# Performance work log

Measured on AMD Instinct MI355X. Metric: run time of the kernel, lower is better.

## Reference

```python
import jax, jax.numpy as jnp
import numpy as np

LAMBDA_DRO = 0.1
EPSILON = 0.5
EPS = 1e-8

N, M, D, K = 2048, 4096, 512, 1000


def _cosine_matrix(a, b):
    # a: [N, d], b: [M, d] -> [N, M] cosine similarity via normalize + GEMM
    an = a / jnp.maximum(jnp.linalg.norm(a, axis=1, keepdims=True), EPS)
    bn = b / jnp.maximum(jnp.linalg.norm(b, axis=1, keepdims=True), EPS)
    return an @ bn.T


def setup_inputs() -> dict:
    key = jax.random.key(0)
    k = jax.random.split(key, 7)
    return {
        "ptr_features": jax.random.normal(k[0], (N, D), dtype=jnp.float32),
        "ptr_logits": jax.random.normal(k[1], (N, K), dtype=jnp.float32),
        "ptr_labels": jax.random.randint(k[2], (N,), 0, K),
        "nu_features": jax.random.normal(k[3], (M, D), dtype=jnp.float32),
        "nu_logits": jax.random.normal(k[4], (M, K), dtype=jnp.float32),
        "nu_labels": jax.random.randint(k[5], (M,), 0, K),
        "classifier_weights": jax.random.normal(k[6], (K, D), dtype=jnp.float32),
    }


def reference(ptr_features, ptr_logits, ptr_labels, nu_features, nu_logits,
              nu_labels, classifier_weights):
    # per-sample CE loss on nu (hard labels)
    log_probs = jax.nn.log_softmax(nu_logits, axis=1)          # [M, K]
    nu_losses = -jnp.take_along_axis(log_probs, nu_labels[:, None], axis=1)[:, 0]  # [M]

    # transport costs
    C_X = 1.0 - _cosine_matrix(ptr_features, nu_features)       # [N, M]
    ptr_emb = classifier_weights[ptr_labels]                    # [N, d]
    nu_emb = classifier_weights[nu_labels]                      # [M, d]
    C_Y = 1.0 - _cosine_matrix(ptr_emb, nu_emb)                 # [N, M]
    C_total = C_X + C_Y

    # worst-case distribution Q^lambda
    exponent = (nu_losses[None, :] - LAMBDA_DRO * C_total) / (LAMBDA_DRO * EPSILON + EPS)
    exponent = exponent - jnp.max(exponent, axis=1, keepdims=True)
    exp_terms = jnp.exp(exponent)                               # [N, M]
    weights = exp_terms / (jnp.sum(exp_terms, axis=1, keepdims=True) + EPS)
    probs = jnp.mean(weights, axis=0)                           # [M]
    probs = probs / (jnp.sum(probs) + EPS)

    dro_loss = jnp.sum(probs * nu_losses)
    total_loss = dro_loss  # semantic_loss = 0 (no moco inputs)
    return (total_loss, dro_loss, probs, jnp.mean(C_total), jnp.mean(C_X), jnp.mean(C_Y))
```

## Files before the change

kernel.cpp:

```cpp
#include <hip/hip_runtime.h>
#include <math.h>

#define N_PTR 2048
#define M_NU  4096
#define DIM   512
#define KCLS  1000
#define KPAD  1024

static constexpr float LAMBDA_ = 0.1f;
static constexpr float EPS_ = 1e-8f;
static constexpr float INV_DENOM = 1.0f / (0.1f * 0.5f + 1e-8f);

typedef short short8 __attribute__((ext_vector_type(8)));
typedef unsigned short u16x8 __attribute__((ext_vector_type(8)));
typedef float f32x4 __attribute__((ext_vector_type(4)));

__device__ __forceinline__ unsigned short f2bf(float x) {
  unsigned u = __float_as_uint(x);
  u += 0x7fff + ((u >> 16) & 1);
  return (unsigned short)(u >> 16);
}
__device__ __forceinline__ float bf2f(unsigned short h) {
  return __uint_as_float(((unsigned)h) << 16);
}

__device__ __forceinline__ void gload16(const void* g, void* l) {
  __builtin_amdgcn_global_load_lds(
      (const __attribute__((address_space(1))) unsigned int*)g,
      (__attribute__((address_space(3))) unsigned int*)l, 16, 0, 0);
}

__device__ __forceinline__ float blk_reduce_sum(float v, float* red) {
  #pragma unroll
  for (int off = 32; off > 0; off >>= 1) v += __shfl_down(v, off);
  __syncthreads();
  if ((threadIdx.x & 63) == 0) red[threadIdx.x >> 6] = v;
  __syncthreads();
  return red[0] + red[1] + red[2] + red[3];
}

__device__ __forceinline__ float blk_reduce_max(float v, float* red) {
  #pragma unroll
  for (int off = 32; off > 0; off >>= 1) v = fmaxf(v, __shfl_down(v, off));
  __syncthreads();
  if ((threadIdx.x & 63) == 0) red[threadIdx.x >> 6] = v;
  __syncthreads();
  return fmaxf(fmaxf(red[0], red[1]), fmaxf(red[2], red[3]));
}

__global__ __launch_bounds__(256) void prep_kernel(
    const float* __restrict__ ptr_f, const float* __restrict__ nu_f,
    const float* __restrict__ cls_f, const float* __restrict__ logits,
    const int* __restrict__ labels, unsigned short* __restrict__ An,
    unsigned short* __restrict__ Bn, unsigned short* __restrict__ Cn,
    float* __restrict__ losses) {
  __shared__ float red[4];
  int b = blockIdx.x;
  if (b < 1792) {
    int gid = b * 256 + threadIdx.x;
    int row = gid >> 6, lane = gid & 63;
    const float* src; unsigned short* dst; int lrow; int in_rows;
    if (row < N_PTR)             { src = ptr_f; dst = An; lrow = row;                in_rows = N_PTR; }
    else if (row < N_PTR + M_NU) { src = nu_f;  dst = Bn; lrow = row - N_PTR;        in_rows = M_NU; }
    else                         { src = cls_f; dst = Cn; lrow = row - N_PTR - M_NU; in_rows = KCLS; }
    u16x8 ov;
    if (lrow < in_rows) {
      const float4* rp = (const float4*)(src + (size_t)lrow * DIM);
      float4 a = rp[lane * 2], bq = rp[lane * 2 + 1];
      float v[8] = {a.x, a.y, a.z, a.w, bq.x, bq.y, bq.z, bq.w};
      float s = 0.f;
      #pragma unroll
      for (int j = 0; j < 8; ++j) s = fmaf(v[j], v[j], s);
      #pragma unroll
      for (int off = 32; off > 0; off >>= 1) s += __shfl_xor(s, off);
      float inv = 1.0f / fmaxf(sqrtf(s), EPS_);
      #pragma unroll
      for (int j = 0; j < 8; ++j) ov[j] = f2bf(v[j] * inv);
    } else {
      #pragma unroll
      for (int j = 0; j < 8; ++j) ov[j] = 0;
    }
    *(u16x8*)(dst + (size_t)lrow * DIM + lane * 8) = ov;
  } else {
    int row = b - 1792;
    int tid = threadIdx.x;
    const float* x = logits + (size_t)row * KCLS;
    const float4* x4 = (const float4*)x;
    float4 v = make_float4(0.f, 0.f, 0.f, 0.f);
    float mx_loc = -INFINITY;
    if (tid < 250) {
      v = x4[tid];
      mx_loc = fmaxf(fmaxf(v.x, v.y), fmaxf(v.z, v.w));
    }
    float mx = blk_reduce_max(mx_loc, red);
    float se_loc = 0.f;
    if (tid < 250)
      se_loc = __expf(v.x - mx) + __expf(v.y - mx) + __expf(v.z - mx) + __expf(v.w - mx);
    float se = blk_reduce_sum(se_loc, red);
    if (tid == 0) losses[row] = mx + logf(se) - x[labels[row]];
  }
}

template <int BM, int MODE>
__global__ __launch_bounds__(256) void mfma_gemm(
    const unsigned short* __restrict__ A, const unsigned short* __restrict__ B,
    unsigned short* __restrict__ Gfb, unsigned short* __restrict__ Tb,
    const int* __restrict__ pl, const int* __restrict__ nl,
    const float* __restrict__ nu_loss, unsigned* __restrict__ gbits,
    float* __restrict__ pr, float* __restrict__ pr2,
    float* __restrict__ s_part, float* __restrict__ gy_part, int ldc) {
  constexpr int FR = BM / 32;
  constexpr int WSPAN = BM / 2;
  __shared__ unsigned short Alds[BM * 64];
  __shared__ unsigned short Blds[BM * 64];
  __shared__ float red[4];
  const int tid = threadIdx.x;
  const int w = tid >> 6, lane = tid & 63;
  const int brow = blockIdx.y * BM, bcol = blockIdx.x * BM;
  const int wr = w >> 1, wc = w & 1;

  if (MODE == 0 && blockIdx.x == 0 && blockIdx.y == 0) {
    float mloc = 0.f;
    for (int i = tid; i < M_NU; i += 256) mloc = fmaxf(mloc, nu_loss[i]);
    float mx = blk_reduce_max(mloc, red);
    if (tid == 0) *gbits = __float_as_uint(mx);
    __syncthreads();
  }

  const int sr = lane >> 3;
  const int sc = lane & 7;
  const int schunk = (sc ^ sr) * 8;

  f32x4 acc[FR][FR] = {};

  for (int k0 = 0; k0 < DIM; k0 += 64) {
    #pragma unroll
    for (int i = 0; i < FR; ++i) {
      int j = w * FR + i;
      int r = j * 8 + sr;
      gload16(A + (size_t)(brow + r) * DIM + k0 + schunk, (char*)Alds + j * 1024);
      gload16(B + (size_t)(bcol + r) * DIM + k0 + schunk, (char*)Blds + j * 1024);
    }
    __syncthreads();
    #pragma unroll
    for (int kk = 0; kk < 2; ++kk) {
      const int koff = kk * 64 + (lane >> 4) * 16;
      short8 af[FR], bfr[FR];
      #pragma unroll
      for (int mi = 0; mi < FR; ++mi) {
        int r = wr * WSPAN + mi * 16 + (lane & 15);
        af[mi] = *(const short8*)((const char*)Alds + r * 128 + (koff ^ ((r & 7) << 4)));
      }
      #pragma unroll
      for (int ni = 0; ni < FR; ++ni) {
        int r = wc * WSPAN + ni * 16 + (lane & 15);
        bfr[ni] = *(const short8*)((const char*)Blds + r * 128 + (koff ^ ((r & 7) << 4)));
      }
      #pragma unroll
      for (int mi = 0; mi < FR; ++mi)
        #pragma unroll
        for (int ni = 0; ni < FR; ++ni)
          acc[mi][ni] = __builtin_amdgcn_mfma_f32_16x16x32_bf16(af[mi], bfr[ni], acc[mi][ni], 0, 0, 0);
    }
    __syncthreads();
  }

  if (MODE == 0) {
    #pragma unroll
    for (int mi = 0; mi < FR; ++mi)
      #pragma unroll
      for (int ni = 0; ni < FR; ++ni)
        #pragma unroll
        for (int j = 0; j < 4; ++j) {
          int row = brow + wr * WSPAN + mi * 16 + (lane >> 4) * 4 + j;
          int col = bcol + wc * WSPAN + ni * 16 + (lane & 15);
          Gfb[(size_t)row * ldc + col] = f2bf(acc[mi][ni][j]);
        }
  } else {
    const float gmax = __uint_as_float(*gbits);
    const float fac = LAMBDA_ * INV_DENOM;
    int cols[FR]; float a_r[FR]; float loss_r[FR]; int nl_r[FR];
    #pragma unroll
    for (int ni = 0; ni < FR; ++ni) {
      cols[ni]  = bcol + wc * WSPAN + ni * 16 + (lane & 15);
      loss_r[ni] = nu_loss[cols[ni]];
      a_r[ni]   = (loss_r[ni] - gmax - 2.f * LAMBDA_) * INV_DENOM;
      nl_r[ni]  = nl[cols[ni]];
    }
    float s_acc = 0.f, gy_acc = 0.f;
    #pragma unroll
    for (int mi = 0; mi < FR; ++mi) {
      #pragma unroll
      for (int j = 0; j < 4; ++j) {
        int row = brow + wr * WSPAN + mi * 16 + (lane >> 4) * 4 + j;
        const unsigned short* Grow = Gfb + (size_t)pl[row] * KPAD;
        float rowacc = 0.f, rowacc2 = 0.f;
        #pragma unroll
        for (int ni = 0; ni < FR; ++ni) {
          float s  = acc[mi][ni][j];
          float gy = bf2f(Grow[nl_r[ni]]);
          float e  = fmaf(fac, s + gy, a_r[ni]);
          float t  = __expf(e);
          unsigned short tb = f2bf(t);
          Tb[(size_t)row * ldc + cols[ni]] = tb;
          float tt = bf2f(tb);
          rowacc  += tt;
          rowacc2 += tt * loss_r[ni];
          s_acc += s; gy_acc += gy;
        }
        #pragma unroll
        for (int off = 1; off < 16; off <<= 1) {
          rowacc  += __shfl_xor(rowacc, off);
          rowacc2 += __shfl_xor(rowacc2, off);
        }
        if ((lane & 15) == 0) {
          pr [(size_t)(blockIdx.x * 2 + wc) * N_PTR + row] = rowacc;
          pr2[(size_t)(blockIdx.x * 2 + wc) * N_PTR + row] = rowacc2;
        }
      }
    }
    float stot = blk_reduce_sum(s_acc, red);
    float gtot = blk_reduce_sum(gy_acc, red);
    if (tid == 0) {
      int bid = blockIdx.y * gridDim.x + blockIdx.x;
      s_part[bid] = stot; gy_part[bid] = gtot;
    }
  }
}

__global__ __launch_bounds__(256) void colpass_td_kernel(
    const unsigned short* __restrict__ Tb, const float* __restrict__ pr,
    const float* __restrict__ pr2, float* __restrict__ partial,
    float* __restrict__ T_part, float* __restrict__ D_part) {
  __shared__ float sh[64];
  int b = blockIdx.x, tid = threadIdx.x;
  if (b < 256) {
    int bx = b & 7, by = b >> 3;
    int m0 = bx * 512 + tid * 2;
    int n0 = by * 64;
    if (tid < 64) {
      float rs = 0.f;
      #pragma unroll 4
      for (int cb = 0; cb < 64; ++cb) rs += pr[(size_t)cb * N_PTR + n0 + tid];
      sh[tid] = 1.0f / (rs + EPS_);
    }
    __syncthreads();
    float a0 = 0.f, a1 = 0.f;
    #pragma unroll 4
    for (int i = 0; i < 64; ++i) {
      unsigned tv = *(const unsigned*)(Tb + (size_t)(n0 + i) * M_NU + m0);
      float wv = sh[i];
      a0 = fmaf(bf2f((unsigned short)(tv & 0xffffu)), wv, a0);
      a1 = fmaf(bf2f((unsigned short)(tv >> 16)), wv, a1);
    }
    *(float2*)(partial + (size_t)by * M_NU + m0) = make_float2(a0, a1);
  } else {
    int n = (b - 256) * 128 + (tid & 127);
    float tl = 0.f, dl = 0.f;
    if (tid < 128) {
      float rs = 0.f, wl = 0.f;
      #pragma unroll 4
      for (int cb = 0; cb < 64; ++cb) {
        rs += pr [(size_t)cb * N_PTR + n];
        wl += pr2[(size_t)cb * N_PTR + n];
      }
      float wi = 1.0f / (rs + EPS_);
      tl = rs * wi; dl = wl * wi;
    }
    __syncthreads();
    #pragma unroll
    for (int off = 32; off > 0; off >>= 1) { tl += __shfl_down(tl, off); dl += __shfl_down(dl, off); }
    if ((tid & 63) == 0) { sh[tid >> 6] = tl; sh[4 + (tid >> 6)] = dl; }
    __syncthreads();
    if (tid == 0) {
      T_part[b - 256] = sh[0] + sh[1] + sh[2] + sh[3];
      D_part[b - 256] = sh[4] + sh[5] + sh[6] + sh[7];
    }
  }
}

__global__ __launch_bounds__(256) void final_kernel(const float* __restrict__ partial,
    const float* __restrict__ T_part, const float* __restrict__ D_part,
    const float* __restrict__ s_part, const float* __restrict__ gy_part,
    float* __restrict__ out) {
  __shared__ float red[4];
  int b = blockIdx.x, tid = threadIdx.x;
  float T = 0.f;
  #pragma unroll
  for (int i = 0; i < 16; ++i) T += T_part[i];
  float scale = (1.0f / (float)N_PTR) / (T / (float)N_PTR + EPS_);
  if (b < 16) {
    int m = b * 256 + tid;
    float raw = 0.f;
    #pragma unroll
    for (int c = 0; c < 32; ++c) raw += partial[(size_t)c * M_NU + m];
    out[2 + m] = raw * scale;
  } else {
    float D = 0.f;
    #pragma unroll
    for (int i = 0; i < 16; ++i) D += D_part[i];
    float ls = 0.f, lg = 0.f;
    for (int i = tid; i < 512; i += 256) { ls += s_part[i]; lg += gy_part[i]; }
    float S  = blk_reduce_sum(ls, red);
    float Gy = blk_reduce_sum(lg, red);
    if (tid == 0) {
      float dro = D * scale;
      const float invNM = 1.0f / ((float)N_PTR * (float)M_NU);
      float mcx = 1.f - S * invNM;
      float mcy = 1.f - Gy * invNM;
      out[0] = dro;
      out[1] = dro;
      out[2 + M_NU] = mcx + mcy;
      out[3 + M_NU] = mcx;
      out[4 + M_NU] = mcy;
    }
  }
}

extern "C" void kernel_launch(void* const* d_in, const int* in_sizes, int n_in,
                              void* d_out, int out_size, void* d_ws, size_t ws_size,
                              hipStream_t stream) {
  const float* ptr_feat = (const float*)d_in[0];
  const int*   ptr_lab  = (const int*)d_in[2];
  const float* nu_feat  = (const float*)d_in[3];
  const float* nu_log   = (const float*)d_in[4];
  const int*   nu_lab   = (const int*)d_in[5];
  const float* cls_w    = (const float*)d_in[6];
  float* out = (float*)d_out;

  char* base = (char*)d_ws;
  unsigned short* Tb  = (unsigned short*)base;
  unsigned short* Gfb = (unsigned short*)(base + 16u * 1024 * 1024);
  unsigned short* An  = (unsigned short*)(base + 18u * 1024 * 1024);
  unsigned short* Bn  = (unsigned short*)(base + 20u * 1024 * 1024);
  unsigned short* Cn  = (unsigned short*)(base + 24u * 1024 * 1024);
  float* fb           = (float*)(base + 25u * 1024 * 1024);
  float* nloss   = fb;
  unsigned* gbits= (unsigned*)(nloss + 4096);
  float* pr      = nloss + 4096 + 64;
  float* pr2     = pr  + 64 * N_PTR;
  float* partial = pr2 + 64 * N_PTR;
  float* s_part  = partial + 32 * M_NU;
  float* gy_part = s_part + 512;
  float* T_part  = gy_part + 512;
  float* D_part  = T_part + 16;

  prep_kernel<<<dim3(1792 + M_NU), 256, 0, stream>>>(
      ptr_feat, nu_feat, cls_w, nu_log, nu_lab, An, Bn, Cn, nloss);
  mfma_gemm<64, 0><<<dim3(KPAD / 64, KPAD / 64), 256, 0, stream>>>(
      Cn, Cn, Gfb, nullptr, nullptr, nullptr, nloss, gbits,
      nullptr, nullptr, nullptr, nullptr, KPAD);
  mfma_gemm<128, 1><<<dim3(M_NU / 128, N_PTR / 128), 256, 0, stream>>>(
      An, Bn, Gfb, Tb, ptr_lab, nu_lab, nloss, gbits,
      pr, pr2, s_part, gy_part, M_NU);
  colpass_td_kernel<<<dim3(272), 256, 0, stream>>>(Tb, pr, pr2, partial, T_part, D_part);
  final_kernel<<<dim3(17), 256, 0, stream>>>(partial, T_part, D_part, s_part, gy_part, out);
}
```

Before: 62.79 us.

## Transpose MFMA output layout for vectorized stores and use wave-per-row softmax

The MFMA operands are swapped so each lane holds four consecutive columns of one row. The GEMM epilogues can then write packed 4-element bf16 stores instead of scattered 2-byte stores, and each row's partial sums need only two cross-lane shuffles. Separately, the per-row cross-entropy now runs one wavefront per row, four rows per block, using only wave shuffles and no block barriers. The cost is more per-lane registers for the per-column loss and label arrays, and gather reads of Gfb that are now per-row rather than per-column.

Result: slower. 79.67 us (+26.9%).

```diff
diff --git a/kernel.cpp b/kernel.cpp
--- a/kernel.cpp
+++ b/kernel.cpp
@@ -13,6 +13,7 @@
 
 typedef short short8 __attribute__((ext_vector_type(8)));
 typedef unsigned short u16x8 __attribute__((ext_vector_type(8)));
+typedef unsigned short u16x4 __attribute__((ext_vector_type(4)));
 typedef float f32x4 __attribute__((ext_vector_type(4)));
 
 __device__ __forceinline__ unsigned short f2bf(float x) {
@@ -54,10 +55,10 @@
     const int* __restrict__ labels, unsigned short* __restrict__ An,
     unsigned short* __restrict__ Bn, unsigned short* __restrict__ Cn,
     float* __restrict__ losses) {
-  __shared__ float red[4];
   int b = blockIdx.x;
+  int tid = threadIdx.x;
   if (b < 1792) {
-    int gid = b * 256 + threadIdx.x;
+    int gid = b * 256 + tid;
     int row = gid >> 6, lane = gid & 63;
     const float* src; unsigned short* dst; int lrow; int in_rows;
     if (row < N_PTR)             { src = ptr_f; dst = An; lrow = row;                in_rows = N_PTR; }
@@ -82,22 +83,27 @@
     }
     *(u16x8*)(dst + (size_t)lrow * DIM + lane * 8) = ov;
   } else {
-    int row = b - 1792;
-    int tid = threadIdx.x;
-    const float* x = logits + (size_t)row * KCLS;
-    const float4* x4 = (const float4*)x;
-    float4 v = make_float4(0.f, 0.f, 0.f, 0.f);
-    float mx_loc = -INFINITY;
-    if (tid < 250) {
-      v = x4[tid];
-      mx_loc = fmaxf(fmaxf(v.x, v.y), fmaxf(v.z, v.w));
-    }
-    float mx = blk_reduce_max(mx_loc, red);
-    float se_loc = 0.f;
-    if (tid < 250)
-      se_loc = __expf(v.x - mx) + __expf(v.y - mx) + __expf(v.z - mx) + __expf(v.w - mx);
-    float se = blk_reduce_sum(se_loc, red);
-    if (tid == 0) losses[row] = mx + logf(se) - x[labels[row]];
+    int row = (b - 1792) * 4 + (tid >> 6);
+    int lane = tid & 63;
+    const float4* x4 = (const float4*)(logits + (size_t)row * KCLS);
+    float4 v0 = x4[lane], v1 = x4[lane + 64], v2 = x4[lane + 128];
+    bool has3 = lane < 58;
+    float4 v3 = has3 ? x4[lane + 192] : make_float4(0.f, 0.f, 0.f, 0.f);
+    float mx = fmaxf(fmaxf(fmaxf(v0.x, v0.y), fmaxf(v0.z, v0.w)),
+               fmaxf(fmaxf(fmaxf(v1.x, v1.y), fmaxf(v1.z, v1.w)),
+                     fmaxf(fmaxf(v2.x, v2.y), fmaxf(v2.z, v2.w))));
+    if (has3) mx = fmaxf(mx, fmaxf(fmaxf(v3.x, v3.y), fmaxf(v3.z, v3.w)));
+    #pragma unroll
+    for (int off = 32; off > 0; off >>= 1) mx = fmaxf(mx, __shfl_xor(mx, off));
+    float se = __expf(v0.x - mx) + __expf(v0.y - mx) + __expf(v0.z - mx) + __expf(v0.w - mx)
+             + __expf(v1.x - mx) + __expf(v1.y - mx) + __expf(v1.z - mx) + __expf(v1.w - mx)
+             + __expf(v2.x - mx) + __expf(v2.y - mx) + __expf(v2.z - mx) + __expf(v2.w - mx);
+    if (has3)
+      se += __expf(v3.x - mx) + __expf(v3.y - mx) + __expf(v3.z - mx) + __expf(v3.w - mx);
+    #pragma unroll
+    for (int off = 32; off > 0; off >>= 1) se += __shfl_xor(se, off);
+    if (lane == 0)
+      losses[row] = mx + logf(se) - logits[(size_t)row * KCLS + labels[row]];
   }
 }
 
@@ -160,63 +166,66 @@
       for (int mi = 0; mi < FR; ++mi)
         #pragma unroll
         for (int ni = 0; ni < FR; ++ni)
-          acc[mi][ni] = __builtin_amdgcn_mfma_f32_16x16x32_bf16(af[mi], bfr[ni], acc[mi][ni], 0, 0, 0);
+          acc[mi][ni] = __builtin_amdgcn_mfma_f32_16x16x32_bf16(bfr[ni], af[mi], acc[mi][ni], 0, 0, 0);
     }
     __syncthreads();
   }
 
   if (MODE == 0) {
     #pragma unroll
-    for (int mi = 0; mi < FR; ++mi)
-      #pragma unroll
-      for (int ni = 0; ni < FR; ++ni)
+    for (int mi = 0; mi < FR; ++mi) {
+      int n = brow + wr * WSPAN + mi * 16 + (lane & 15);
+      #pragma unroll
+      for (int ni = 0; ni < FR; ++ni) {
+        int mb = bcol + wc * WSPAN + ni * 16 + ((lane >> 4) << 2);
+        u16x4 o;
         #pragma unroll
-        for (int j = 0; j < 4; ++j) {
-          int row = brow + wr * WSPAN + mi * 16 + (lane >> 4) * 4 + j;
-          int col = bcol + wc * WSPAN + ni * 16 + (lane & 15);
-          Gfb[(size_t)row * ldc + col] = f2bf(acc[mi][ni][j]);
-        }
+        for (int j = 0; j < 4; ++j) o[j] = f2bf(acc[mi][ni][j]);
+        *(u16x4*)(Gfb + (size_t)n * ldc + mb) = o;
+      }
+    }
   } else {
     const float gmax = __uint_as_float(*gbits);
     const float fac = LAMBDA_ * INV_DENOM;
-    int cols[FR]; float a_r[FR]; float loss_r[FR]; int nl_r[FR];
-    #pragma unroll
-    for (int ni = 0; ni < FR; ++ni) {
-      cols[ni]  = bcol + wc * WSPAN + ni * 16 + (lane & 15);
-      loss_r[ni] = nu_loss[cols[ni]];
-      a_r[ni]   = (loss_r[ni] - gmax - 2.f * LAMBDA_) * INV_DENOM;
-      nl_r[ni]  = nl[cols[ni]];
-    }
+    float a_r[FR][4]; float l_r[FR][4]; int nl_r[FR][4];
+    #pragma unroll
+    for (int ni = 0; ni < FR; ++ni)
+      #pragma unroll
+      for (int j = 0; j < 4; ++j) {
+        int m = bcol + wc * WSPAN + ni * 16 + ((lane >> 4) << 2) + j;
+        float l = nu_loss[m];
+        l_r[ni][j]  = l;
+        a_r[ni][j]  = (l - gmax - 2.f * LAMBDA_) * INV_DENOM;
+        nl_r[ni][j] = nl[m];
+      }
     float s_acc = 0.f, gy_acc = 0.f;
     #pragma unroll
     for (int mi = 0; mi < FR; ++mi) {
-      #pragma unroll
-      for (int j = 0; j < 4; ++j) {
-        int row = brow + wr * WSPAN + mi * 16 + (lane >> 4) * 4 + j;
-        const unsigned short* Grow = Gfb + (size_t)pl[row] * KPAD;
-        float rowacc = 0.f, rowacc2 = 0.f;
+      int n = brow + wr * WSPAN + mi * 16 + (lane & 15);
+      const unsigned short* Grow = Gfb + (size_t)pl[n] * KPAD;
+      float ra = 0.f, ra2 = 0.f;
+      #pragma unroll
+      for (int ni = 0; ni < FR; ++ni) {
+        int mb = bcol + wc * WSPAN + ni * 16 + ((lane >> 4) << 2);
+        u16x4 o;
         #pragma unroll
-        for (int ni = 0; ni < FR; ++ni) {
+        for (int j = 0; j < 4; ++j) {
           float s  = acc[mi][ni][j];
-          float gy = bf2f(Grow[nl_r[ni]]);
-          float e  = fmaf(fac, s + gy, a_r[ni]);
-          float t  = __expf(e);
-          unsigned short tb = f2bf(t);
-          Tb[(size_t)row * ldc + cols[ni]] = tb;
-          float tt = bf2f(tb);
-          rowacc  += tt;
-          rowacc2 += tt * loss_r[ni];
+          float gy = bf2f(Grow[nl_r[ni][j]]);
+          float t  = __expf(fmaf(fac, s + gy, a_r[ni][j]));
+          o[j] = f2bf(t);
+          float tt = bf2f(o[j]);
+          ra  += tt;
+          ra2 += tt * l_r[ni][j];
           s_acc += s; gy_acc += gy;
         }
-        #pragma unroll
-        for (int off = 1; off < 16; off <<= 1) {
-          rowacc  += __shfl_xor(rowacc, off);
-          rowacc2 += __shfl_xor(rowacc2, off);
-        }
-        if ((lane & 15) == 0) {
-          pr [(size_t)(blockIdx.x * 2 + wc) * N_PTR + row] = rowacc;
-          pr2[(size_t)(blockIdx.x * 2 + wc) * N_PTR + row] = rowacc2;
-        }
+        *(u16x4*)(Tb + (size_t)n * ldc + mb) = o;
+      }
+      ra  += __shfl_xor(ra, 16);  ra  += __shfl_xor(ra, 32);
+      ra2 += __shfl_xor(ra2, 16); ra2 += __shfl_xor(ra2, 32);
+      if (lane < 16) {
+        pr [(size_t)(blockIdx.x * 2 + wc) * N_PTR + n] = ra;
+        pr2[(size_t)(blockIdx.x * 2 + wc) * N_PTR + n] = ra2;
       }
     }
     float stot = blk_reduce_sum(s_acc, red);
@@ -345,7 +354,7 @@
   float* T_part  = gy_part + 512;
   float* D_part  = T_part + 16;
 
-  prep_kernel<<<dim3(1792 + M_NU), 256, 0, stream>>>(
+  prep_kernel<<<dim3(1792 + M_NU / 4), 256, 0, stream>>>(
       ptr_feat, nu_feat, cls_w, nu_log, nu_lab, An, Bn, Cn, nloss);
   mfma_gemm<64, 0><<<dim3(KPAD / 64, KPAD / 64), 256, 0, stream>>>(
       Cn, Cn, Gfb, nullptr, nullptr, nullptr, nloss, gbits,
```

## Split big GEMM epilogue into a separate row pass and compute means via column sums

Applied to the files above, without the earlier changes.

The big feature GEMM now only writes bf16 similarities with vectorized transposed stores. A new row-pass kernel reads them back with the class-embedding row cached in LDS, computes the exp terms and row sums, and overwrites them in place. The means of C_X and C_Y are now computed from column sums of the normalized embeddings (sum of dot products equals the dot product of sums), in extra blocks of the small GEMM, replacing the per-element accumulation. This drops gather and exp work from the GEMM epilogue, but it adds one more kernel launch and an extra read and write of the N×M bf16 matrix.

Result: slower. 102.5 us (+63.3%).

```diff
diff --git a/kernel.cpp b/kernel.cpp
--- a/kernel.cpp
+++ b/kernel.cpp
@@ -13,6 +13,7 @@
 
 typedef short short8 __attribute__((ext_vector_type(8)));
 typedef unsigned short u16x8 __attribute__((ext_vector_type(8)));
+typedef unsigned short u16x4 __attribute__((ext_vector_type(4)));
 typedef float f32x4 __attribute__((ext_vector_type(4)));
 
 __device__ __forceinline__ unsigned short f2bf(float x) {
@@ -56,8 +57,9 @@
     float* __restrict__ losses) {
   __shared__ float red[4];
   int b = blockIdx.x;
+  int tid = threadIdx.x;
   if (b < 1792) {
-    int gid = b * 256 + threadIdx.x;
+    int gid = b * 256 + tid;
     int row = gid >> 6, lane = gid & 63;
     const float* src; unsigned short* dst; int lrow; int in_rows;
     if (row < N_PTR)             { src = ptr_f; dst = An; lrow = row;                in_rows = N_PTR; }
@@ -83,7 +85,6 @@
     *(u16x8*)(dst + (size_t)lrow * DIM + lane * 8) = ov;
   } else {
     int row = b - 1792;
-    int tid = threadIdx.x;
     const float* x = logits + (size_t)row * KCLS;
     const float4* x4 = (const float4*)x;
     float4 v = make_float4(0.f, 0.f, 0.f, 0.f);
@@ -101,31 +102,54 @@
   }
 }
 
-template <int BM, int MODE>
-__global__ __launch_bounds__(256) void mfma_gemm(
+template <int BM, int GX, int EXTRA>
+__global__ __launch_bounds__(256) void gemm_kernel(
     const unsigned short* __restrict__ A, const unsigned short* __restrict__ B,
-    unsigned short* __restrict__ Gfb, unsigned short* __restrict__ Tb,
+    unsigned short* __restrict__ C, int ldc,
+    const unsigned short* __restrict__ An, const unsigned short* __restrict__ Bn,
+    const unsigned short* __restrict__ Cn,
     const int* __restrict__ pl, const int* __restrict__ nl,
-    const float* __restrict__ nu_loss, unsigned* __restrict__ gbits,
-    float* __restrict__ pr, float* __restrict__ pr2,
-    float* __restrict__ s_part, float* __restrict__ gy_part, int ldc) {
+    const float* __restrict__ nloss, float* __restrict__ csum_part,
+    unsigned* __restrict__ gbits) {
   constexpr int FR = BM / 32;
   constexpr int WSPAN = BM / 2;
+  constexpr int NTILES = GX * 16;
+  const int b = blockIdx.x;
+  const int tid = threadIdx.x;
+
+  if (EXTRA && b >= NTILES) {
+    int j = b - NTILES;
+    __shared__ float red[4];
+    if (j == 96) {
+      float mloc = 0.f;
+      for (int i = tid; i < M_NU; i += 256) mloc = fmaxf(mloc, nloss[i]);
+      float mx = blk_reduce_max(mloc, red);
+      if (tid == 0) *gbits = __float_as_uint(mx);
+      return;
+    }
+    const unsigned short* basep; const int* idx = nullptr; int n0;
+    if (j < 16)      { basep = An; n0 = j * 128; }
+    else if (j < 48) { basep = Bn; n0 = (j - 16) * 128; }
+    else if (j < 64) { basep = Cn; idx = pl; n0 = (j - 48) * 128; }
+    else             { basep = Cn; idx = nl; n0 = (j - 64) * 128; }
+    float a0 = 0.f, a1 = 0.f;
+    for (int i = 0; i < 128; ++i) {
+      int rr = n0 + i;
+      const unsigned short* rowp = basep + (size_t)(idx ? idx[rr] : rr) * DIM;
+      unsigned v = *(const unsigned*)(rowp + tid * 2);
+      a0 += bf2f((unsigned short)(v & 0xffffu));
+      a1 += bf2f((unsigned short)(v >> 16));
+    }
+    csum_part[(size_t)j * DIM + tid * 2]     = a0;
+    csum_part[(size_t)j * DIM + tid * 2 + 1] = a1;
+    return;
+  }
+
   __shared__ unsigned short Alds[BM * 64];
   __shared__ unsigned short Blds[BM * 64];
-  __shared__ float red[4];
-  const int tid = threadIdx.x;
   const int w = tid >> 6, lane = tid & 63;
-  const int brow = blockIdx.y * BM, bcol = blockIdx.x * BM;
+  const int bcol = (b % GX) * BM, brow = (b / GX) * BM;
   const int wr = w >> 1, wc = w & 1;
-
-  if (MODE == 0 && blockIdx.x == 0 && blockIdx.y == 0) {
-    float mloc = 0.f;
-    for (int i = tid; i < M_NU; i += 256) mloc = fmaxf(mloc, nu_loss[i]);
-    float mx = blk_reduce_max(mloc, red);
-    if (tid == 0) *gbits = __float_as_uint(mx);
-    __syncthreads();
-  }
 
   const int sr = lane >> 3;
   const int sc = lane & 7;
@@ -160,134 +184,122 @@
       for (int mi = 0; mi < FR; ++mi)
         #pragma unroll
         for (int ni = 0; ni < FR; ++ni)
-          acc[mi][ni] = __builtin_amdgcn_mfma_f32_16x16x32_bf16(af[mi], bfr[ni], acc[mi][ni], 0, 0, 0);
+          acc[mi][ni] = __builtin_amdgcn_mfma_f32_16x16x32_bf16(bfr[ni], af[mi], acc[mi][ni], 0, 0, 0);
     }
     __syncthreads();
   }
 
-  if (MODE == 0) {
-    #pragma unroll
-    for (int mi = 0; mi < FR; ++mi)
-      #pragma unroll
-      for (int ni = 0; ni < FR; ++ni)
-        #pragma unroll
-        for (int j = 0; j < 4; ++j) {
-          int row = brow + wr * WSPAN + mi * 16 + (lane >> 4) * 4 + j;
-          int col = bcol + wc * WSPAN + ni * 16 + (lane & 15);
-          Gfb[(size_t)row * ldc + col] = f2bf(acc[mi][ni][j]);
-        }
-  } else {
-    const float gmax = __uint_as_float(*gbits);
-    const float fac = LAMBDA_ * INV_DENOM;
-    int cols[FR]; float a_r[FR]; float loss_r[FR]; int nl_r[FR];
+  #pragma unroll
+  for (int mi = 0; mi < FR; ++mi) {
+    int n = brow + wr * WSPAN + mi * 16 + (lane & 15);
     #pragma unroll
     for (int ni = 0; ni < FR; ++ni) {
-      cols[ni]  = bcol + wc * WSPAN + ni * 16 + (lane & 15);
-      loss_r[ni] = nu_loss[cols[ni]];
-      a_r[ni]   = (loss_r[ni] - gmax - 2.f * LAMBDA_) * INV_DENOM;
-      nl_r[ni]  = nl[cols[ni]];
-    }
-    float s_acc = 0.f, gy_acc = 0.f;
-    #pragma unroll
-    for (int mi = 0; mi < FR; ++mi) {
-      #pragma unroll
-      for (int j = 0; j < 4; ++j) {
-        int row = brow + wr * WSPAN + mi * 16 + (lane >> 4) * 4 + j;
-        const unsigned short* Grow = Gfb + (size_t)pl[row] * KPAD;
-        float rowacc = 0.f, rowacc2 = 0.f;
-        #pragma unroll
-        for (int ni = 0; ni < FR; ++ni) {
-          float s  = acc[mi][ni][j];
-          float gy = bf2f(Grow[nl_r[ni]]);
-          float e  = fmaf(fac, s + gy, a_r[ni]);
-          float t  = __expf(e);
-          unsigned short tb = f2bf(t);
-          Tb[(size_t)row * ldc + cols[ni]] = tb;
-          float tt = bf2f(tb);
-          rowacc  += tt;
-          rowacc2 += tt * loss_r[ni];
-          s_acc += s; gy_acc += gy;
-        }
-        #pragma unroll
-        for (int off = 1; off < 16; off <<= 1) {
-          rowacc  += __shfl_xor(rowacc, off);
-          rowacc2 += __shfl_xor(rowacc2, off);
-        }
-        if ((lane & 15) == 0) {
-          pr [(size_t)(blockIdx.x * 2 + wc) * N_PTR + row] = rowacc;
-          pr2[(size_t)(blockIdx.x * 2 + wc) * N_PTR + row] = rowacc2;
-        }
-      }
-    }
-    float stot = blk_reduce_sum(s_acc, red);
-    float gtot = blk_reduce_sum(gy_acc, red);
-    if (tid == 0) {
-      int bid = blockIdx.y * gridDim.x + blockIdx.x;
-      s_part[bid] = stot; gy_part[bid] = gtot;
-    }
-  }
-}
-
-__global__ __launch_bounds__(256) void colpass_td_kernel(
-    const unsigned short* __restrict__ Tb, const float* __restrict__ pr,
-    const float* __restrict__ pr2, float* __restrict__ partial,
-    float* __restrict__ T_part, float* __restrict__ D_part) {
-  __shared__ float sh[64];
+      int mb = bcol + wc * WSPAN + ni * 16 + ((lane >> 4) << 2);
+      u16x4 o;
+      #pragma unroll
+      for (int j = 0; j < 4; ++j) o[j] = f2bf(acc[mi][ni][j]);
+      *(u16x4*)(C + (size_t)n * ldc + mb) = o;
+    }
+  }
+}
+
+__global__ __launch_bounds__(256) void rowpass_kernel(
+    unsigned short* __restrict__ Sb, const unsigned short* __restrict__ Gfb,
+    const int* __restrict__ pl, const int* __restrict__ nl,
+    const float* __restrict__ nloss, const unsigned* __restrict__ gbits,
+    float* __restrict__ winv, float* __restrict__ trow, float* __restrict__ drow) {
+  __shared__ unsigned short Gld[4][KPAD];
+  const int wv = threadIdx.x >> 6, lane = threadIdx.x & 63;
+  const int n = blockIdx.x * 4 + wv;
+  const float gmax = __uint_as_float(*gbits);
+  const float fac = LAMBDA_ * INV_DENOM;
+  const float csh = gmax + 2.f * LAMBDA_;
+  const unsigned short* Grow = Gfb + (size_t)pl[n] * KPAD;
+  *(u16x8*)(&Gld[wv][lane * 16])     = *(const u16x8*)(Grow + lane * 16);
+  *(u16x8*)(&Gld[wv][lane * 16 + 8]) = *(const u16x8*)(Grow + lane * 16 + 8);
+  __syncthreads();
+  unsigned short* Srow = Sb + (size_t)n * M_NU;
+  float rs = 0.f, rl = 0.f;
+  #pragma unroll
+  for (int it = 0; it < 4; ++it) {
+    const int m0 = it * 1024 + lane * 16;
+    u16x8 s0 = *(const u16x8*)(Srow + m0);
+    u16x8 s1 = *(const u16x8*)(Srow + m0 + 8);
+    int4 n0v = *(const int4*)(nl + m0);
+    int4 n1v = *(const int4*)(nl + m0 + 4);
+    int4 n2v = *(const int4*)(nl + m0 + 8);
+    int4 n3v = *(const int4*)(nl + m0 + 12);
+    float4 l0 = *(const float4*)(nloss + m0);
+    float4 l1 = *(const float4*)(nloss + m0 + 4);
+    float4 l2 = *(const float4*)(nloss + m0 + 8);
+    float4 l3 = *(const float4*)(nloss + m0 + 12);
+    const int nli[16] = {n0v.x, n0v.y, n0v.z, n0v.w, n1v.x, n1v.y, n1v.z, n1v.w,
+                         n2v.x, n2v.y, n2v.z, n2v.w, n3v.x, n3v.y, n3v.z, n3v.w};
+    const float li[16] = {l0.x, l0.y, l0.z, l0.w, l1.x, l1.y, l1.z, l1.w,
+                          l2.x, l2.y, l2.z, l2.w, l3.x, l3.y, l3.z, l3.w};
+    u16x8 t0, t1;
+    #pragma unroll
+    for (int j = 0; j < 8; ++j) {
+      float gy = bf2f(Gld[wv][nli[j]]);
+      float t  = __expf(fmaf(fac, bf2f(s0[j]) + gy, (li[j] - csh) * INV_DENOM));
+      t0[j] = f2bf(t);
+      float tt = bf2f(t0[j]);
+      rs += tt; rl += tt * li[j];
+    }
+    #pragma unroll
+    for (int j = 0; j < 8; ++j) {
+      float gy = bf2f(Gld[wv][nli[8 + j]]);
+      float t  = __expf(fmaf(fac, bf2f(s1[j]) + gy, (li[8 + j] - csh) * INV_DENOM));
+      t1[j] = f2bf(t);
+      float tt = bf2f(t1[j]);
+      rs += tt; rl += tt * li[8 + j];
+    }
+    *(u16x8*)(Srow + m0)     = t0;
+    *(u16x8*)(Srow + m0 + 8) = t1;
+  }
+  #pragma unroll
+  for (int off = 32; off > 0; off >>= 1) {
+    rs += __shfl_xor(rs, off);
+    rl += __shfl_xor(rl, off);
+  }
+  if (lane == 0) {
+    float wi = 1.0f / (rs + EPS_);
+    winv[n] = wi;
+    trow[n] = rs * wi;
+    drow[n] = rl * wi;
+  }
+}
+
+__global__ __launch_bounds__(256) void colpass_kernel(
+    const unsigned short* __restrict__ Tb, const float* __restrict__ winv,
+    float* __restrict__ partial) {
+  __shared__ float w[64];
   int b = blockIdx.x, tid = threadIdx.x;
-  if (b < 256) {
-    int bx = b & 7, by = b >> 3;
-    int m0 = bx * 512 + tid * 2;
-    int n0 = by * 64;
-    if (tid < 64) {
-      float rs = 0.f;
-      #pragma unroll 4
-      for (int cb = 0; cb < 64; ++cb) rs += pr[(size_t)cb * N_PTR + n0 + tid];
-      sh[tid] = 1.0f / (rs + EPS_);
-    }
-    __syncthreads();
-    float a0 = 0.f, a1 = 0.f;
-    #pragma unroll 4
-    for (int i = 0; i < 64; ++i) {
-      unsigned tv = *(const unsigned*)(Tb + (size_t)(n0 + i) * M_NU + m0);
-      float wv = sh[i];
-      a0 = fmaf(bf2f((unsigned short)(tv & 0xffffu)), wv, a0);
-      a1 = fmaf(bf2f((unsigned short)(tv >> 16)), wv, a1);
-    }
-    *(float2*)(partial + (size_t)by * M_NU + m0) = make_float2(a0, a1);
-  } else {
-    int n = (b - 256) * 128 + (tid & 127);
-    float tl = 0.f, dl = 0.f;
-    if (tid < 128) {
-      float rs = 0.f, wl = 0.f;
-      #pragma unroll 4
-      for (int cb = 0; cb < 64; ++cb) {
-        rs += pr [(size_t)cb * N_PTR + n];
-        wl += pr2[(size_t)cb * N_PTR + n];
-      }
-      float wi = 1.0f / (rs + EPS_);
-      tl = rs * wi; dl = wl * wi;
-    }
-    __syncthreads();
-    #pragma unroll
-    for (int off = 32; off > 0; off >>= 1) { tl += __shfl_down(tl, off); dl += __shfl_down(dl, off); }
-    if ((tid & 63) == 0) { sh[tid >> 6] = tl; sh[4 + (tid >> 6)] = dl; }
-    __syncthreads();
-    if (tid == 0) {
-      T_part[b - 256] = sh[0] + sh[1] + sh[2] + sh[3];
-      D_part[b - 256] = sh[4] + sh[5] + sh[6] + sh[7];
-    }
-  }
-}
-
-__global__ __launch_bounds__(256) void final_kernel(const float* __restrict__ partial,
-    const float* __restrict__ T_part, const float* __restrict__ D_part,
-    const float* __restrict__ s_part, const float* __restrict__ gy_part,
+  int bx = b & 7, by = b >> 3;
+  int m0 = bx * 512 + tid * 2;
+  int n0 = by * 64;
+  if (tid < 64) w[tid] = winv[n0 + tid];
+  __syncthreads();
+  float a0 = 0.f, a1 = 0.f;
+  #pragma unroll 4
+  for (int i = 0; i < 64; ++i) {
+    unsigned tv = *(const unsigned*)(Tb + (size_t)(n0 + i) * M_NU + m0);
+    float wv = w[i];
+    a0 = fmaf(bf2f((unsigned short)(tv & 0xffffu)), wv, a0);
+    a1 = fmaf(bf2f((unsigned short)(tv >> 16)), wv, a1);
+  }
+  *(float2*)(partial + (size_t)by * M_NU + m0) = make_float2(a0, a1);
+}
+
+__global__ __launch_bounds__(256) void final_kernel(
+    const float* __restrict__ partial, const float* __restrict__ trow,
+    const float* __restrict__ drow, const float* __restrict__ csum_part,
     float* __restrict__ out) {
   __shared__ float red[4];
   int b = blockIdx.x, tid = threadIdx.x;
-  float T = 0.f;
-  #pragma unroll
-  for (int i = 0; i < 16; ++i) T += T_part[i];
+  float lt = 0.f;
+  for (int i = tid; i < N_PTR; i += 256) lt += trow[i];
+  float T = blk_reduce_sum(lt, red);
   float scale = (1.0f / (float)N_PTR) / (T / (float)N_PTR + EPS_);
   if (b < 16) {
     int m = b * 256 + tid;
@@ -296,18 +308,30 @@
     for (int c = 0; c < 32; ++c) raw += partial[(size_t)c * M_NU + m];
     out[2 + m] = raw * scale;
   } else {
-    float D = 0.f;
-    #pragma unroll
-    for (int i = 0; i < 16; ++i) D += D_part[i];
-    float ls = 0.f, lg = 0.f;
-    for (int i = tid; i < 512; i += 256) { ls += s_part[i]; lg += gy_part[i]; }
-    float S  = blk_reduce_sum(ls, red);
-    float Gy = blk_reduce_sum(lg, red);
+    float ld = 0.f;
+    for (int i = tid; i < N_PTR; i += 256) ld += drow[i];
+    float D = blk_reduce_sum(ld, red);
+    float lx = 0.f, ly = 0.f;
+    for (int c = tid; c < DIM; c += 256) {
+      float sA = 0.f, sB = 0.f, sPe = 0.f, sQe = 0.f;
+      #pragma unroll 4
+      for (int p = 0; p < 16; ++p)  sA  += csum_part[(size_t)p * DIM + c];
+      #pragma unroll 4
+      for (int p = 16; p < 48; ++p) sB  += csum_part[(size_t)p * DIM + c];
+      #pragma unroll 4
+      for (int p = 48; p < 64; ++p) sPe += csum_part[(size_t)p * DIM + c];
+      #pragma unroll 4
+      for (int p = 64; p < 96; ++p) sQe += csum_part[(size_t)p * DIM + c];
+      lx = fmaf(sA, sB, lx);
+      ly = fmaf(sPe, sQe, ly);
+    }
+    float dX = blk_reduce_sum(lx, red);
+    float dY = blk_reduce_sum(ly, red);
     if (tid == 0) {
       float dro = D * scale;
       const float invNM = 1.0f / ((float)N_PTR * (float)M_NU);
-      float mcx = 1.f - S * invNM;
-      float mcy = 1.f - Gy * invNM;
+      float mcx = 1.f - dX * invNM;
+      float mcy = 1.f - dY * invNM;
       out[0] = dro;
       out[1] = dro;
       out[2 + M_NU] = mcx + mcy;
@@ -329,30 +353,29 @@
   float* out = (float*)d_out;
 
   char* base = (char*)d_ws;
-  unsigned short* Tb  = (unsigned short*)base;
+  unsigned short* Sb  = (unsigned short*)base;
   unsigned short* Gfb = (unsigned short*)(base + 16u * 1024 * 1024);
   unsigned short* An  = (unsigned short*)(base + 18u * 1024 * 1024);
   unsigned short* Bn  = (unsigned short*)(base + 20u * 1024 * 1024);
   unsigned short* Cn  = (unsigned short*)(base + 24u * 1024 * 1024);
   float* fb           = (float*)(base + 25u * 1024 * 1024);
-  float* nloss   = fb;
-  unsigned* gbits= (unsigned*)(nloss + 4096);
-  float* pr      = nloss + 4096 + 64;
-  float* pr2     = pr  + 64 * N_PTR;
-  float* partial = pr2 + 64 * N_PTR;
-  float* s_part  = partial + 32 * M_NU;
-  float* gy_part = s_part + 512;
-  float* T_part  = gy_part + 512;
-  float* D_part  = T_part + 16;
+  float* nloss     = fb;
+  unsigned* gbits  = (unsigned*)(nloss + 4096);
+  float* winv      = nloss + 4096 + 64;
+  float* trow      = winv + N_PTR;
+  float* drow      = trow + N_PTR;
+  float* partial   = drow + N_PTR;
+  float* csum_part = partial + 32 * M_NU;
 
   prep_kernel<<<dim3(1792 + M_NU), 256, 0, stream>>>(
       ptr_feat, nu_feat, cls_w, nu_log, nu_lab, An, Bn, Cn, nloss);
-  mfma_gemm<64, 0><<<dim3(KPAD / 64, KPAD / 64), 256, 0, stream>>>(
-      Cn, Cn, Gfb, nullptr, nullptr, nullptr, nloss, gbits,
-      nullptr, nullptr, nullptr, nullptr, KPAD);
-  mfma_gemm<128, 1><<<dim3(M_NU / 128, N_PTR / 128), 256, 0, stream>>>(
-      An, Bn, Gfb, Tb, ptr_lab, nu_lab, nloss, gbits,
-      pr, pr2, s_part, gy_part, M_NU);
-  colpass_td_kernel<<<dim3(272), 256, 0, stream>>>(Tb, pr, pr2, partial, T_part, D_part);
-  final_kernel<<<dim3(17), 256, 0, stream>>>(partial, T_part, D_part, s_part, gy_part, out);
-}
+  gemm_kernel<128, 32, 0><<<dim3(512), 256, 0, stream>>>(
+      An, Bn, Sb, M_NU, nullptr, nullptr, nullptr, nullptr, nullptr,
+      nullptr, nullptr, nullptr);
+  gemm_kernel<64, 16, 1><<<dim3(256 + 97), 256, 0, stream>>>(
+      Cn, Cn, Gfb, KPAD, An, Bn, Cn, ptr_lab, nu_lab, nloss, csum_part, gbits);
+  rowpass_kernel<<<dim3(N_PTR / 4), 256, 0, stream>>>(
+      Sb, Gfb, ptr_lab, nu_lab, nloss, gbits, winv, trow, drow);
+  colpass_kernel<<<dim3(256), 256, 0, stream>>>(Sb, winv, partial);
+  final_kernel<<<dim3(17), 256, 0, stream>>>(partial, trow, drow, csum_part, out);
+}
```

## Replace main fused GEMM with 512-thread, 8-wave kernel using smaller per-wave tiles

Applied to the files above, without the earlier changes.

The main cosine GEMM with fused exp epilogue moves to a dedicated kernel with 512 threads (8 waves, each holding a 64x32 sub-tile) on the same 128x128 block tile. Each wave now keeps fewer accumulator fragments, which lowers register pressure and is meant to allow more resident waves to hide memory and epilogue latency. Because there are now 4 column waves per block, the per-row partial sums double to 128 slices, so the column pass reads twice as many partials. The costs are more LDS fragment reads per MFMA and more synchronisation across waves.

After: 66.33 us. +5.6%, slower.

```diff
diff --git a/kernel.cpp b/kernel.cpp
--- a/kernel.cpp
+++ b/kernel.cpp
@@ -46,6 +46,18 @@
   if ((threadIdx.x & 63) == 0) red[threadIdx.x >> 6] = v;
   __syncthreads();
   return fmaxf(fmaxf(red[0], red[1]), fmaxf(red[2], red[3]));
+}
+
+__device__ __forceinline__ float blk512_reduce_sum(float v, float* red) {
+  #pragma unroll
+  for (int off = 32; off > 0; off >>= 1) v += __shfl_down(v, off);
+  __syncthreads();
+  if ((threadIdx.x & 63) == 0) red[threadIdx.x >> 6] = v;
+  __syncthreads();
+  float s = 0.f;
+  #pragma unroll
+  for (int i = 0; i < 8; ++i) s += red[i];
+  return s;
 }
 
 __global__ __launch_bounds__(256) void prep_kernel(
@@ -176,55 +188,109 @@
           int col = bcol + wc * WSPAN + ni * 16 + (lane & 15);
           Gfb[(size_t)row * ldc + col] = f2bf(acc[mi][ni][j]);
         }
-  } else {
-    const float gmax = __uint_as_float(*gbits);
-    const float fac = LAMBDA_ * INV_DENOM;
-    int cols[FR]; float a_r[FR]; float loss_r[FR]; int nl_r[FR];
-    #pragma unroll
-    for (int ni = 0; ni < FR; ++ni) {
-      cols[ni]  = bcol + wc * WSPAN + ni * 16 + (lane & 15);
-      loss_r[ni] = nu_loss[cols[ni]];
-      a_r[ni]   = (loss_r[ni] - gmax - 2.f * LAMBDA_) * INV_DENOM;
-      nl_r[ni]  = nl[cols[ni]];
-    }
-    float s_acc = 0.f, gy_acc = 0.f;
-    #pragma unroll
-    for (int mi = 0; mi < FR; ++mi) {
-      #pragma unroll
-      for (int j = 0; j < 4; ++j) {
-        int row = brow + wr * WSPAN + mi * 16 + (lane >> 4) * 4 + j;
-        const unsigned short* Grow = Gfb + (size_t)pl[row] * KPAD;
-        float rowacc = 0.f, rowacc2 = 0.f;
+  }
+}
+
+__global__ __launch_bounds__(512, 4) void sgemm8_kernel(
+    const unsigned short* __restrict__ A, const unsigned short* __restrict__ B,
+    const unsigned short* __restrict__ Gfb, unsigned short* __restrict__ Tb,
+    const int* __restrict__ pl, const int* __restrict__ nl,
+    const float* __restrict__ nu_loss, const unsigned* __restrict__ gbits,
+    float* __restrict__ pr, float* __restrict__ pr2,
+    float* __restrict__ s_part, float* __restrict__ gy_part) {
+  __shared__ unsigned short Alds[128 * 64];
+  __shared__ unsigned short Blds[128 * 64];
+  __shared__ float red[8];
+  const int tid = threadIdx.x;
+  const int w = tid >> 6, lane = tid & 63;
+  const int brow = blockIdx.y * 128, bcol = blockIdx.x * 128;
+  const int wr = w >> 2, wc = w & 3;
+
+  const int sr = lane >> 3;
+  const int sc = lane & 7;
+  const int schunk = (sc ^ sr) * 8;
+
+  f32x4 acc[4][2] = {};
+
+  for (int k0 = 0; k0 < DIM; k0 += 64) {
+    #pragma unroll
+    for (int i = 0; i < 2; ++i) {
+      int j = w * 2 + i;
+      int r = j * 8 + sr;
+      gload16(A + (size_t)(brow + r) * DIM + k0 + schunk, (char*)Alds + j * 1024);
+      gload16(B + (size_t)(bcol + r) * DIM + k0 + schunk, (char*)Blds + j * 1024);
+    }
+    __syncthreads();
+    #pragma unroll
+    for (int kk = 0; kk < 2; ++kk) {
+      const int koff = kk * 64 + (lane >> 4) * 16;
+      short8 af[4], bfr[2];
+      #pragma unroll
+      for (int mi = 0; mi < 4; ++mi) {
+        int r = wr * 64 + mi * 16 + (lane & 15);
+        af[mi] = *(const short8*)((const char*)Alds + r * 128 + (koff ^ ((r & 7) << 4)));
+      }
+      #pragma unroll
+      for (int ni = 0; ni < 2; ++ni) {
+        int r = wc * 32 + ni * 16 + (lane & 15);
+        bfr[ni] = *(const short8*)((const char*)Blds + r * 128 + (koff ^ ((r & 7) << 4)));
+      }
+      #pragma unroll
+      for (int mi = 0; mi < 4; ++mi)
         #pragma unroll
-        for (int ni = 0; ni < FR; ++ni) {
-          float s  = acc[mi][ni][j];
-          float gy = bf2f(Grow[nl_r[ni]]);
-          float e  = fmaf(fac, s + gy, a_r[ni]);
-          float t  = __expf(e);
-          unsigned short tb = f2bf(t);
-          Tb[(size_t)row * ldc + cols[ni]] = tb;
-          float tt = bf2f(tb);
-          rowacc  += tt;
-          rowacc2 += tt * loss_r[ni];
-          s_acc += s; gy_acc += gy;
-        }
-        #pragma unroll
-        for (int off = 1; off < 16; off <<= 1) {
-          rowacc  += __shfl_xor(rowacc, off);
-          rowacc2 += __shfl_xor(rowacc2, off);
-        }
-        if ((lane & 15) == 0) {
-          pr [(size_t)(blockIdx.x * 2 + wc) * N_PTR + row] = rowacc;
-          pr2[(size_t)(blockIdx.x * 2 + wc) * N_PTR + row] = rowacc2;
-        }
-      }
-    }
-    float stot = blk_reduce_sum(s_acc, red);
-    float gtot = blk_reduce_sum(gy_acc, red);
-    if (tid == 0) {
-      int bid = blockIdx.y * gridDim.x + blockIdx.x;
-      s_part[bid] = stot; gy_part[bid] = gtot;
-    }
+        for (int ni = 0; ni < 2; ++ni)
+          acc[mi][ni] = __builtin_amdgcn_mfma_f32_16x16x32_bf16(af[mi], bfr[ni], acc[mi][ni], 0, 0, 0);
+    }
+    __syncthreads();
+  }
+
+  const float gmax = __uint_as_float(*gbits);
+  const float fac = LAMBDA_ * INV_DENOM;
+  int cols[2]; float a_r[2]; float loss_r[2]; int nl_r[2];
+  #pragma unroll
+  for (int ni = 0; ni < 2; ++ni) {
+    cols[ni]   = bcol + wc * 32 + ni * 16 + (lane & 15);
+    loss_r[ni] = nu_loss[cols[ni]];
+    a_r[ni]    = (loss_r[ni] - gmax - 2.f * LAMBDA_) * INV_DENOM;
+    nl_r[ni]   = nl[cols[ni]];
+  }
+  float s_acc = 0.f, gy_acc = 0.f;
+  #pragma unroll
+  for (int mi = 0; mi < 4; ++mi) {
+    #pragma unroll
+    for (int j = 0; j < 4; ++j) {
+      int row = brow + wr * 64 + mi * 16 + (lane >> 4) * 4 + j;
+      const unsigned short* Grow = Gfb + (size_t)pl[row] * KPAD;
+      float rowacc = 0.f, rowacc2 = 0.f;
+      #pragma unroll
+      for (int ni = 0; ni < 2; ++ni) {
+        float s  = acc[mi][ni][j];
+        float gy = bf2f(Grow[nl_r[ni]]);
+        float e  = fmaf(fac, s + gy, a_r[ni]);
+        float t  = __expf(e);
+        unsigned short tb = f2bf(t);
+        Tb[(size_t)row * M_NU + cols[ni]] = tb;
+        float tt = bf2f(tb);
+        rowacc  += tt;
+        rowacc2 += tt * loss_r[ni];
+        s_acc += s; gy_acc += gy;
+      }
+      #pragma unroll
+      for (int off = 1; off < 16; off <<= 1) {
+        rowacc  += __shfl_xor(rowacc, off);
+        rowacc2 += __shfl_xor(rowacc2, off);
+      }
+      if ((lane & 15) == 0) {
+        pr [(size_t)(blockIdx.x * 4 + wc) * N_PTR + row] = rowacc;
+        pr2[(size_t)(blockIdx.x * 4 + wc) * N_PTR + row] = rowacc2;
+      }
+    }
+  }
+  float stot = blk512_reduce_sum(s_acc, red);
+  float gtot = blk512_reduce_sum(gy_acc, red);
+  if (tid == 0) {
+    int bid = blockIdx.y * gridDim.x + blockIdx.x;
+    s_part[bid] = stot; gy_part[bid] = gtot;
   }
 }
 
@@ -241,7 +307,7 @@
     if (tid < 64) {
       float rs = 0.f;
       #pragma unroll 4
-      for (int cb = 0; cb < 64; ++cb) rs += pr[(size_t)cb * N_PTR + n0 + tid];
+      for (int cb = 0; cb < 128; ++cb) rs += pr[(size_t)cb * N_PTR + n0 + tid];
       sh[tid] = 1.0f / (rs + EPS_);
     }
     __syncthreads();
@@ -260,7 +326,7 @@
     if (tid < 128) {
       float rs = 0.f, wl = 0.f;
       #pragma unroll 4
-      for (int cb = 0; cb < 64; ++cb) {
+      for (int cb = 0; cb < 128; ++cb) {
         rs += pr [(size_t)cb * N_PTR + n];
         wl += pr2[(size_t)cb * N_PTR + n];
       }
@@ -338,8 +404,8 @@
   float* nloss   = fb;
   unsigned* gbits= (unsigned*)(nloss + 4096);
   float* pr      = nloss + 4096 + 64;
-  float* pr2     = pr  + 64 * N_PTR;
-  float* partial = pr2 + 64 * N_PTR;
+  float* pr2     = pr  + 128 * N_PTR;
+  float* partial = pr2 + 128 * N_PTR;
   float* s_part  = partial + 32 * M_NU;
   float* gy_part = s_part + 512;
   float* T_part  = gy_part + 512;
@@ -350,9 +416,9 @@
   mfma_gemm<64, 0><<<dim3(KPAD / 64, KPAD / 64), 256, 0, stream>>>(
       Cn, Cn, Gfb, nullptr, nullptr, nullptr, nloss, gbits,
       nullptr, nullptr, nullptr, nullptr, KPAD);
-  mfma_gemm<128, 1><<<dim3(M_NU / 128, N_PTR / 128), 256, 0, stream>>>(
+  sgemm8_kernel<<<dim3(M_NU / 128, N_PTR / 128), 512, 0, stream>>>(
       An, Bn, Gfb, Tb, ptr_lab, nu_lab, nloss, gbits,
-      pr, pr2, s_part, gy_part, M_NU);
+      pr, pr2, s_part, gy_part);
   colpass_td_kernel<<<dim3(272), 256, 0, stream>>>(Tb, pr, pr2, partial, T_part, D_part);
   final_kernel<<<dim3(17), 256, 0, stream>>>(partial, T_part, D_part, s_part, gy_part, out);
 }
```
